# Kernel tuning notes

Hardware: AMD Instinct MI355X
Metric: run time of the kernel (lower is better)

## Reference

```python
import jax, jax.numpy as jnp
import numpy as np

B, HW, NTGT, C = 2, 4096, 4096, 512
H, KNN = 8, 32
DH = C // H
SCALE = DH ** -0.5


def setup_inputs() -> dict:
    key = jax.random.key(0)
    ks = jax.random.split(key, 12)
    s = 1.0 / np.sqrt(C)
    return {
        "src": jax.random.normal(ks[0], (B, HW, C), jnp.float32),
        "tgt": jax.random.normal(ks[1], (B, NTGT, C), jnp.float32),
        "indices": jax.random.randint(ks[2], (B, HW, KNN), 0, NTGT, jnp.int64),
        "weights": jax.random.normal(ks[3], (B, HW, KNN), jnp.float32),
        "Wq": jax.random.normal(ks[4], (C, C), jnp.float32) * s,
        "bq": jnp.zeros((C,), jnp.float32),
        "Wk": jax.random.normal(ks[5], (C, C), jnp.float32) * s,
        "bk": jnp.zeros((C,), jnp.float32),
        "Wv": jax.random.normal(ks[6], (C, C), jnp.float32) * s,
        "bv": jnp.zeros((C,), jnp.float32),
        "Wo": jax.random.normal(ks[7], (C, C), jnp.float32) * s,
        "bo": jnp.zeros((C,), jnp.float32),
    }


def reference(src, tgt, indices, weights, Wq, bq, Wk, bk, Wv, bv, Wo, bo):
    b, hw, c = src.shape
    # projections -> (b, H, seq, dh)
    q = (src @ Wq + bq).reshape(b, hw, H, DH).transpose(0, 2, 1, 3)
    k = (tgt @ Wk + bk).reshape(b, -1, H, DH).transpose(0, 2, 1, 3)
    v = (tgt @ Wv + bv).reshape(b, -1, H, DH).transpose(0, 2, 1, 3)
    # gather epipolar neighbors: per batch, kb[:, idx] -> (H, hw, KNN, dh)
    gather = jax.vmap(lambda xb, ib: xb[:, ib])
    k_g = gather(k, indices)  # (b, H, hw, KNN, dh)
    v_g = gather(v, indices)  # (b, H, hw, KNN, dh)
    logits = jnp.einsum("bhqd,bhqkd->bhqk", q, k_g) * SCALE
    logits = logits + weights[:, None]  # broadcast over heads
    attn = jax.nn.softmax(logits, axis=-1)
    out = jnp.einsum("bhqk,bhqkd->bhqd", attn, v_g)
    out = out.transpose(0, 2, 1, 3).reshape(b, hw, c)
    return out @ Wo + bo
```

## Files before the change

kernel.cpp:

```cpp
#include <hip/hip_runtime.h>
#include <hip/hip_bf16.h>
#include <stdint.h>
#include <type_traits>

#define B_    2
#define HW_   4096
#define NTGT_ 4096
#define C_    512
#define H_    8
#define KNN_  32
#define DH_   64
#define M_    (B_ * HW_)

typedef unsigned short ushort_t;
typedef __bf16 bf16x8 __attribute__((ext_vector_type(8)));
typedef float floatx4 __attribute__((ext_vector_type(4)));

__device__ __forceinline__ float b2f(ushort_t u) {
    union { uint32_t i; float f; } x;
    x.i = ((uint32_t)u) << 16;
    return x.f;
}
__device__ __forceinline__ ushort_t f2b(float f) {
    union { float f; uint32_t i; } x;
    x.f = f;
    uint32_t r = x.i + 0x7fffu + ((x.i >> 16) & 1u);
    return (ushort_t)(r >> 16);
}
__device__ __forceinline__ uint32_t pk2(float x, float y) {
    union { __hip_bfloat162 h2; uint32_t u; } c;
    c.h2 = __float22bfloat162_rn(make_float2(x, y));
    return c.u;
}
__device__ __forceinline__ uint4 pack8(const float4& a, const float4& b) {
    return make_uint4(pk2(a.x, a.y), pk2(a.z, a.w), pk2(b.x, b.y), pk2(b.z, b.w));
}

__global__ __launch_bounds__(256) void transpose_inplace4_f32(
    float* W0, float* W1, float* W2, float* W3) {
    __shared__ float ta[32][33];
    __shared__ float tb[32][33];

    float* W = (blockIdx.y == 0) ? W0 : (blockIdx.y == 1) ? W1
               : (blockIdx.y == 2) ? W2 : W3;

    int p = blockIdx.x;
    int i = 0, acc = 0;
    while (acc + (16 - i) <= p) { acc += 16 - i; ++i; }
    const int j = i + (p - acc);

    const int t = threadIdx.x;
    const int r = t >> 3;
    const int c0 = (t & 7) * 4;

    {
        float4 d = *(const float4*)&W[(size_t)(i * 32 + r) * 512 + j * 32 + c0];
        ta[r][c0 + 0] = d.x; ta[r][c0 + 1] = d.y;
        ta[r][c0 + 2] = d.z; ta[r][c0 + 3] = d.w;
    }
    if (i != j) {
        float4 d = *(const float4*)&W[(size_t)(j * 32 + r) * 512 + i * 32 + c0];
        tb[r][c0 + 0] = d.x; tb[r][c0 + 1] = d.y;
        tb[r][c0 + 2] = d.z; tb[r][c0 + 3] = d.w;
    }
    __syncthreads();

    *(float4*)&W[(size_t)(j * 32 + r) * 512 + i * 32 + c0] =
        make_float4(ta[c0 + 0][r], ta[c0 + 1][r], ta[c0 + 2][r], ta[c0 + 3][r]);
    if (i != j)
        *(float4*)&W[(size_t)(i * 32 + r) * 512 + j * 32 + c0] =
            make_float4(tb[c0 + 0][r], tb[c0 + 1][r], tb[c0 + 2][r], tb[c0 + 3][r]);
}

template <typename AT, typename OT>
__device__ __forceinline__ void gemm_body(const AT* __restrict__ A,
                                          const float* __restrict__ Wt,
                                          const float* __restrict__ bias,
                                          OT* __restrict__ O,
                                          int bm, int bn) {
    __shared__ ushort_t As[128][40];
    __shared__ ushort_t Bs[64][40];

    const int t = threadIdx.x;
    const int lr = t >> 2;
    const int lc = (t & 3) * 8;

    const int lane = t & 63;
    const int wv = t >> 6;
    const int wr = (wv >> 1) * 64;
    const int wc = (wv & 1) * 32;
    const int r16 = lane & 15;
    const int quad = lane >> 4;

    floatx4 acc[4][2] = {};

    for (int kt = 0; kt < 512; kt += 32) {
        uint4 av0, av1, bv0;
        if constexpr (std::is_same<AT, float>::value) {
            const float* p0 = &A[(size_t)(bm + lr) * 512 + kt + lc];
            const float* p1 = &A[(size_t)(bm + lr + 64) * 512 + kt + lc];
            av0 = pack8(*(const float4*)p0, *(const float4*)(p0 + 4));
            av1 = pack8(*(const float4*)p1, *(const float4*)(p1 + 4));
        } else {
            av0 = *(const uint4*)&A[(size_t)(bm + lr) * 512 + kt + lc];
            av1 = *(const uint4*)&A[(size_t)(bm + lr + 64) * 512 + kt + lc];
        }
        {
            const float* p = &Wt[(size_t)(bn + lr) * 512 + kt + lc];
            bv0 = pack8(*(const float4*)p, *(const float4*)(p + 4));
        }
        __syncthreads();
        *(uint4*)&As[lr][lc] = av0;
        *(uint4*)&As[lr + 64][lc] = av1;
        *(uint4*)&Bs[lr][lc] = bv0;
        __syncthreads();

        bf16x8 af[4], bf[2];
#pragma unroll
        for (int i = 0; i < 4; ++i)
            af[i] = *(const bf16x8*)&As[wr + i * 16 + r16][quad * 8];
#pragma unroll
        for (int j = 0; j < 2; ++j)
            bf[j] = *(const bf16x8*)&Bs[wc + j * 16 + r16][quad * 8];
#pragma unroll
        for (int i = 0; i < 4; ++i)
#pragma unroll
            for (int j = 0; j < 2; ++j)
                acc[i][j] = __builtin_amdgcn_mfma_f32_16x16x32_bf16(
                    af[i], bf[j], acc[i][j], 0, 0, 0);
    }

#pragma unroll
    for (int j = 0; j < 2; ++j) {
        const int col = bn + wc + j * 16 + r16;
        const float bj = bias[col];
#pragma unroll
        for (int i = 0; i < 4; ++i) {
            const int row = bm + wr + i * 16 + quad * 4;
#pragma unroll
            for (int r = 0; r < 4; ++r) {
                float v = acc[i][j][r] + bj;
                if constexpr (std::is_same<OT, ushort_t>::value)
                    O[(size_t)(row + r) * 512 + col] = f2b(v);
                else
                    O[(size_t)(row + r) * 512 + col] = v;
            }
        }
    }
}

__global__ __launch_bounds__(256, 4) void gemm_qkv(
    const float* __restrict__ src, const float* __restrict__ tgt,
    const float* __restrict__ WtQ, const float* __restrict__ WtK,
    const float* __restrict__ WtV,
    const float* __restrict__ bq, const float* __restrict__ bk,
    const float* __restrict__ bv,
    ushort_t* __restrict__ Qb, ushort_t* __restrict__ Kb,
    ushort_t* __restrict__ Vb) {
    const int id = blockIdx.x;
    const int xcd = id & 7;
    const int g = id >> 3;
    const int mgrp = g / 24;
    const int r = g % 24;
    const int z = r >> 3;
    const int bn = (r & 7) * 64;
    const int bm = (xcd + 8 * mgrp) * 128;

    const float* A = (z == 0) ? src : tgt;
    const float* Wt = (z == 0) ? WtQ : (z == 1) ? WtK : WtV;
    const float* bias = (z == 0) ? bq : (z == 1) ? bk : bv;
    ushort_t* O = (z == 0) ? Qb : (z == 1) ? Kb : Vb;
    gemm_body<float, ushort_t>(A, Wt, bias, O, bm, bn);
}

template <typename OT>
__global__ __launch_bounds__(256, 4) void gemm_o(const ushort_t* __restrict__ A,
                                                 const float* __restrict__ Wt,
                                                 const float* __restrict__ bias,
                                                 OT* __restrict__ O) {
    const int id = blockIdx.x;
    const int xcd = id & 7;
    const int g = id >> 3;
    const int mgrp = g >> 3;
    const int bn = (g & 7) * 64;
    const int bm = (xcd + 8 * mgrp) * 128;
    gemm_body<ushort_t, OT>(A, Wt, bias, O, bm, bn);
}

#define KVSTRIDE 520
template <typename IT>
__global__ __launch_bounds__(256) void attn_kernel(const ushort_t* Q,
                                                   const ushort_t* __restrict__ K,
                                                   const ushort_t* __restrict__ V,
                                                   const IT* __restrict__ idx,
                                                   const float* __restrict__ wts,
                                                   ushort_t* O) {
    __shared__ float qs[512];
    __shared__ ushort_t kvs[KNN_][KVSTRIDE];
    __shared__ float ps[H_][KNN_];
    __shared__ int idxs[KNN_];
    __shared__ float ws[KNN_];

    const int t = threadIdx.x;
    const int id = blockIdx.x;
    const int xcd = id & 7;
    const int slot = id >> 3;
    const int b = xcd >> 2;
    const int bq = b * HW_ + (xcd & 3) * 1024 + slot;
    const size_t qoff = (size_t)bq * C_;

    {
        uint32_t d = *(const uint32_t*)(Q + qoff + 2 * t);
        qs[2 * t + 0] = b2f((ushort_t)(d & 0xffffu));
        qs[2 * t + 1] = b2f((ushort_t)(d >> 16));
    }
    if (t < KNN_) {
        idxs[t] = (int)idx[(size_t)bq * KNN_ + t];
        ws[t] = wts[(size_t)bq * KNN_ + t];
    }
    __syncthreads();

    const int sr = t >> 3;
    const int sg = (t & 7) * 8;
    {
        const ushort_t* krow = K + ((size_t)(b * NTGT_ + idxs[sr])) * C_;
#pragma unroll
        for (int j = 0; j < 8; ++j)
            *(uint4*)&kvs[sr][sg + j * 64] = *(const uint4*)(krow + sg + j * 64);
    }
    __syncthreads();

    const int h = t >> 5;
    const int n = t & 31;
    const float* qh = qs + h * DH_;
    float dot = 0.f;
#pragma unroll
    for (int j = 0; j < 8; ++j) {
        uint4 kv = *(const uint4*)&kvs[n][h * DH_ + j * 8];
        const int d0 = j * 8;
        dot = fmaf(qh[d0 + 0], b2f((ushort_t)(kv.x & 0xffffu)), dot);
        dot = fmaf(qh[d0 + 1], b2f((ushort_t)(kv.x >> 16)), dot);
        dot = fmaf(qh[d0 + 2], b2f((ushort_t)(kv.y & 0xffffu)), dot);
        dot = fmaf(qh[d0 + 3], b2f((ushort_t)(kv.y >> 16)), dot);
        dot = fmaf(qh[d0 + 4], b2f((ushort_t)(kv.z & 0xffffu)), dot);
        dot = fmaf(qh[d0 + 5], b2f((ushort_t)(kv.z >> 16)), dot);
        dot = fmaf(qh[d0 + 6], b2f((ushort_t)(kv.w & 0xffffu)), dot);
        dot = fmaf(qh[d0 + 7], b2f((ushort_t)(kv.w >> 16)), dot);
    }
    float logit = dot * 0.125f + ws[n];

    float mx = logit;
#pragma unroll
    for (int o = 16; o > 0; o >>= 1) mx = fmaxf(mx, __shfl_xor(mx, o));
    float e = __expf(logit - mx);
    float s = e;
#pragma unroll
    for (int o = 16; o > 0; o >>= 1) s += __shfl_xor(s, o);
    ps[h][n] = e / s;
    __syncthreads();

    {
        const ushort_t* vrow = V + ((size_t)(b * NTGT_ + idxs[sr])) * C_;
#pragma unroll
        for (int j = 0; j < 8; ++j)
            *(uint4*)&kvs[sr][sg + j * 64] = *(const uint4*)(vrow + sg + j * 64);
    }
    __syncthreads();

    const int d2 = (t & 31) * 2;
    float a0 = 0.f, a1 = 0.f;
#pragma unroll 8
    for (int nn = 0; nn < KNN_; ++nn) {
        uint32_t vv = *(const uint32_t*)&kvs[nn][h * DH_ + d2];
        float p = ps[h][nn];
        a0 = fmaf(p, b2f((ushort_t)(vv & 0xffffu)), a0);
        a1 = fmaf(p, b2f((ushort_t)(vv >> 16)), a1);
    }
    *(uint32_t*)(O + qoff + h * DH_ + d2) = pk2(a0, a1);
}

static int elem_bytes(const void* p, size_t n, int dflt) {
    size_t sz = 0;
    hipError_t err = hipPointerGetAttribute(
        &sz, HIP_POINTER_ATTRIBUTE_RANGE_SIZE, (hipDeviceptr_t)(uintptr_t)p);
    if (err == hipSuccess && sz >= n && (sz % n) == 0) {
        size_t b = sz / n;
        if (b == 2 || b == 4 || b == 8) return (int)b;
    }
    return dflt;
}

extern "C" void kernel_launch(void* const* d_in, const int* in_sizes, int n_in,
                              void* d_out, int out_size, void* d_ws, size_t ws_size,
                              hipStream_t stream) {
    const float* src  = (const float*)d_in[0];
    const float* tgt  = (const float*)d_in[1];
    const void*  idxp = d_in[2];
    const float* wtp  = (const float*)d_in[3];
    float* Wq = (float*)d_in[4];  const float* bq = (const float*)d_in[5];
    float* Wk = (float*)d_in[6];  const float* bk = (const float*)d_in[7];
    float* Wv = (float*)d_in[8];  const float* bv = (const float*)d_in[9];
    float* Wo = (float*)d_in[10]; const float* bo = (const float*)d_in[11];

    const size_t NELEM = (size_t)M_ * C_;
    const size_t NIDX  = (size_t)B_ * HW_ * KNN_;

    const int ib = elem_bytes(idxp, NIDX, 4);
    const int ob = elem_bytes(d_out, NELEM, 4);

    dim3 blk(256);

    ushort_t* Qb = (ushort_t*)d_ws;
    ushort_t* Kb = Qb + NELEM;
    ushort_t* Vb = (ushort_t*)d_out;
    ushort_t* Ob = Qb;

    transpose_inplace4_f32<<<dim3(136, 4), blk, 0, stream>>>(Wq, Wk, Wv, Wo);

    gemm_qkv<<<dim3(1536), blk, 0, stream>>>(
        src, tgt, Wq, Wk, Wv, bq, bk, bv, Qb, Kb, Vb);

    if (ib == 8)
        attn_kernel<long long><<<dim3(B_ * HW_), blk, 0, stream>>>(
            Qb, Kb, Vb, (const long long*)idxp, wtp, Ob);
    else
        attn_kernel<int><<<dim3(B_ * HW_), blk, 0, stream>>>(
            Qb, Kb, Vb, (const int*)idxp, wtp, Ob);

    if (ob == 2)
        gemm_o<ushort_t><<<dim3(512), blk, 0, stream>>>(
            Ob, Wo, bo, (ushort_t*)d_out);
    else
        gemm_o<float><<<dim3(512), blk, 0, stream>>>(
            Ob, Wo, bo, (float*)d_out);
}
```

Baseline: 192.7 us.

## Halve GEMM M-tile, prefetch next K-slice in registers, co-issue K/V gathers

The GEMM tile shrinks from 128x64 to 64x64, which doubles the grid size of both the QKV and output projections, and the main loop now register-prefetches the next K-slice while MFMAs run on the current one. In the attention kernel, the gathered V rows are loaded into registers together with the K rows, so their latency overlaps the logit and softmax phase instead of waiting behind a barrier. The trade-offs are more registers per thread and less A-tile reuse per block, which means more global traffic for the weight operand.

New measurement: 282.6 us. +46.7%, slower.

```diff
diff --git a/kernel.cpp b/kernel.cpp
--- a/kernel.cpp
+++ b/kernel.cpp
@@ -78,7 +78,7 @@
                                           const float* __restrict__ bias,
                                           OT* __restrict__ O,
                                           int bm, int bn) {
-    __shared__ ushort_t As[128][40];
+    __shared__ ushort_t As[64][40];
     __shared__ ushort_t Bs[64][40];
 
     const int t = threadIdx.x;
@@ -87,47 +87,55 @@
 
     const int lane = t & 63;
     const int wv = t >> 6;
-    const int wr = (wv >> 1) * 64;
+    const int wr = (wv >> 1) * 32;
     const int wc = (wv & 1) * 32;
     const int r16 = lane & 15;
     const int quad = lane >> 4;
 
-    floatx4 acc[4][2] = {};
+    floatx4 acc[2][2] = {};
+
+    float4 fa0, fa1, fb0, fb1;
+    uint4 ua;
+
+    if constexpr (std::is_same<AT, float>::value) {
+        const float* p = &A[(size_t)(bm + lr) * 512 + lc];
+        fa0 = *(const float4*)p; fa1 = *(const float4*)(p + 4);
+    } else {
+        ua = *(const uint4*)&A[(size_t)(bm + lr) * 512 + lc];
+    }
+    {
+        const float* p = &Wt[(size_t)(bn + lr) * 512 + lc];
+        fb0 = *(const float4*)p; fb1 = *(const float4*)(p + 4);
+    }
 
     for (int kt = 0; kt < 512; kt += 32) {
-        uint4 av0, av1, bv0;
-        if constexpr (std::is_same<AT, float>::value) {
-            const float* p0 = &A[(size_t)(bm + lr) * 512 + kt + lc];
-            const float* p1 = &A[(size_t)(bm + lr + 64) * 512 + kt + lc];
-            av0 = pack8(*(const float4*)p0, *(const float4*)(p0 + 4));
-            av1 = pack8(*(const float4*)p1, *(const float4*)(p1 + 4));
-        } else {
-            av0 = *(const uint4*)&A[(size_t)(bm + lr) * 512 + kt + lc];
-            av1 = *(const uint4*)&A[(size_t)(bm + lr + 64) * 512 + kt + lc];
+        __syncthreads();
+        if constexpr (std::is_same<AT, float>::value)
+            *(uint4*)&As[lr][lc] = pack8(fa0, fa1);
+        else
+            *(uint4*)&As[lr][lc] = ua;
+        *(uint4*)&Bs[lr][lc] = pack8(fb0, fb1);
+        __syncthreads();
+
+        if (kt + 32 < 512) {
+            if constexpr (std::is_same<AT, float>::value) {
+                const float* p = &A[(size_t)(bm + lr) * 512 + kt + 32 + lc];
+                fa0 = *(const float4*)p; fa1 = *(const float4*)(p + 4);
+            } else {
+                ua = *(const uint4*)&A[(size_t)(bm + lr) * 512 + kt + 32 + lc];
+            }
+            const float* p = &Wt[(size_t)(bn + lr) * 512 + kt + 32 + lc];
+            fb0 = *(const float4*)p; fb1 = *(const float4*)(p + 4);
         }
-        {
-            const float* p = &Wt[(size_t)(bn + lr) * 512 + kt + lc];
-            bv0 = pack8(*(const float4*)p, *(const float4*)(p + 4));
-        }
-        __syncthreads();
-        *(uint4*)&As[lr][lc] = av0;
-        *(uint4*)&As[lr + 64][lc] = av1;
-        *(uint4*)&Bs[lr][lc] = bv0;
-        __syncthreads();
-
-        bf16x8 af[4], bf[2];
-#pragma unroll
-        for (int i = 0; i < 4; ++i)
-            af[i] = *(const bf16x8*)&As[wr + i * 16 + r16][quad * 8];
-#pragma unroll
-        for (int j = 0; j < 2; ++j)
-            bf[j] = *(const bf16x8*)&Bs[wc + j * 16 + r16][quad * 8];
-#pragma unroll
-        for (int i = 0; i < 4; ++i)
-#pragma unroll
-            for (int j = 0; j < 2; ++j)
-                acc[i][j] = __builtin_amdgcn_mfma_f32_16x16x32_bf16(
-                    af[i], bf[j], acc[i][j], 0, 0, 0);
+
+        bf16x8 a0 = *(const bf16x8*)&As[wr + r16][quad * 8];
+        bf16x8 a1 = *(const bf16x8*)&As[wr + 16 + r16][quad * 8];
+        bf16x8 b0 = *(const bf16x8*)&Bs[wc + r16][quad * 8];
+        bf16x8 b1 = *(const bf16x8*)&Bs[wc + 16 + r16][quad * 8];
+        acc[0][0] = __builtin_amdgcn_mfma_f32_16x16x32_bf16(a0, b0, acc[0][0], 0, 0, 0);
+        acc[0][1] = __builtin_amdgcn_mfma_f32_16x16x32_bf16(a0, b1, acc[0][1], 0, 0, 0);
+        acc[1][0] = __builtin_amdgcn_mfma_f32_16x16x32_bf16(a1, b0, acc[1][0], 0, 0, 0);
+        acc[1][1] = __builtin_amdgcn_mfma_f32_16x16x32_bf16(a1, b1, acc[1][1], 0, 0, 0);
     }
 
 #pragma unroll
@@ -135,7 +143,7 @@
         const int col = bn + wc + j * 16 + r16;
         const float bj = bias[col];
 #pragma unroll
-        for (int i = 0; i < 4; ++i) {
+        for (int i = 0; i < 2; ++i) {
             const int row = bm + wr + i * 16 + quad * 4;
 #pragma unroll
             for (int r = 0; r < 4; ++r) {
@@ -164,7 +172,7 @@
     const int r = g % 24;
     const int z = r >> 3;
     const int bn = (r & 7) * 64;
-    const int bm = (xcd + 8 * mgrp) * 128;
+    const int bm = (xcd + 8 * mgrp) * 64;
 
     const float* A = (z == 0) ? src : tgt;
     const float* Wt = (z == 0) ? WtQ : (z == 1) ? WtK : WtV;
@@ -183,7 +191,7 @@
     const int g = id >> 3;
     const int mgrp = g >> 3;
     const int bn = (g & 7) * 64;
-    const int bm = (xcd + 8 * mgrp) * 128;
+    const int bm = (xcd + 8 * mgrp) * 64;
     gemm_body<ushort_t, OT>(A, Wt, bias, O, bm, bn);
 }
 
@@ -222,12 +230,14 @@
 
     const int sr = t >> 3;
     const int sg = (t & 7) * 8;
-    {
-        const ushort_t* krow = K + ((size_t)(b * NTGT_ + idxs[sr])) * C_;
-#pragma unroll
-        for (int j = 0; j < 8; ++j)
-            *(uint4*)&kvs[sr][sg + j * 64] = *(const uint4*)(krow + sg + j * 64);
-    }
+    const size_t roff = ((size_t)(b * NTGT_ + idxs[sr])) * C_;
+    uint4 kr[8], vr[8];
+#pragma unroll
+    for (int j = 0; j < 8; ++j) kr[j] = *(const uint4*)(K + roff + sg + j * 64);
+#pragma unroll
+    for (int j = 0; j < 8; ++j) vr[j] = *(const uint4*)(V + roff + sg + j * 64);
+#pragma unroll
+    for (int j = 0; j < 8; ++j) *(uint4*)&kvs[sr][sg + j * 64] = kr[j];
     __syncthreads();
 
     const int h = t >> 5;
@@ -259,12 +269,8 @@
     ps[h][n] = e / s;
     __syncthreads();
 
-    {
-        const ushort_t* vrow = V + ((size_t)(b * NTGT_ + idxs[sr])) * C_;
-#pragma unroll
-        for (int j = 0; j < 8; ++j)
-            *(uint4*)&kvs[sr][sg + j * 64] = *(const uint4*)(vrow + sg + j * 64);
-    }
+#pragma unroll
+    for (int j = 0; j < 8; ++j) *(uint4*)&kvs[sr][sg + j * 64] = vr[j];
     __syncthreads();
 
     const int d2 = (t & 31) * 2;
@@ -317,7 +323,7 @@
 
     transpose_inplace4_f32<<<dim3(136, 4), blk, 0, stream>>>(Wq, Wk, Wv, Wo);
 
-    gemm_qkv<<<dim3(1536), blk, 0, stream>>>(
+    gemm_qkv<<<dim3(3072), blk, 0, stream>>>(
         src, tgt, Wq, Wk, Wv, bq, bk, bv, Qb, Kb, Vb);
 
     if (ib == 8)
@@ -328,9 +334,9 @@
             Qb, Kb, Vb, (const int*)idxp, wtp, Ob);
 
     if (ob == 2)
-        gemm_o<ushort_t><<<dim3(512), blk, 0, stream>>>(
+        gemm_o<ushort_t><<<dim3(1024), blk, 0, stream>>>(
             Ob, Wo, bo, (ushort_t*)d_out);
     else
-        gemm_o<float><<<dim3(512), blk, 0, stream>>>(
+        gemm_o<float><<<dim3(1024), blk, 0, stream>>>(
             Ob, Wo, bo, (float*)d_out);
 }
```

## Pretranspose weights to bf16 workspace, prefetch GEMM tiles, widen QKV N-tile

Applied to the files above, without the earlier changes.

Weights are now transposed and converted to bf16 once into workspace, out of place, instead of being transposed in place as fp32. The GEMM body register-prefetches the next K-slice from global memory while MFMAs run on the current one, which drops one barrier per iteration. The QKV GEMM uses a 128-wide N tile with fewer blocks and launch bounds of 3. The aim is to halve weight traffic, hide load latency and raise reuse of A, at the cost of more registers and lower occupancy.

Measured after the change: 191.7 us. About the same (-0.5%).

```diff
diff --git a/kernel.cpp b/kernel.cpp
--- a/kernel.cpp
+++ b/kernel.cpp
@@ -36,6 +36,35 @@
     return make_uint4(pk2(a.x, a.y), pk2(a.z, a.w), pk2(b.x, b.y), pk2(b.z, b.w));
 }
 
+__global__ __launch_bounds__(256) void transpose_cvt4(
+    const float* __restrict__ W0, const float* __restrict__ W1,
+    const float* __restrict__ W2, const float* __restrict__ W3,
+    ushort_t* __restrict__ T0, ushort_t* __restrict__ T1,
+    ushort_t* __restrict__ T2, ushort_t* __restrict__ T3) {
+    __shared__ float tile[32][33];
+
+    const float* W = (blockIdx.z == 0) ? W0 : (blockIdx.z == 1) ? W1
+                     : (blockIdx.z == 2) ? W2 : W3;
+    ushort_t* T = (blockIdx.z == 0) ? T0 : (blockIdx.z == 1) ? T1
+                  : (blockIdx.z == 2) ? T2 : T3;
+
+    const int k0 = blockIdx.x * 32;
+    const int n0 = blockIdx.y * 32;
+    const int t = threadIdx.x;
+    const int r = t >> 3;
+    const int c0 = (t & 7) * 4;
+
+    float4 d = *(const float4*)&W[(size_t)(k0 + r) * 512 + n0 + c0];
+    tile[r][c0 + 0] = d.x; tile[r][c0 + 1] = d.y;
+    tile[r][c0 + 2] = d.z; tile[r][c0 + 3] = d.w;
+    __syncthreads();
+
+    uint2 o;
+    o.x = pk2(tile[c0 + 0][r], tile[c0 + 1][r]);
+    o.y = pk2(tile[c0 + 2][r], tile[c0 + 3][r]);
+    *(uint2*)&T[(size_t)(n0 + r) * 512 + k0 + c0] = o;
+}
+
 __global__ __launch_bounds__(256) void transpose_inplace4_f32(
     float* W0, float* W1, float* W2, float* W3) {
     __shared__ float ta[32][33];
@@ -72,14 +101,15 @@
             make_float4(tb[c0 + 0][r], tb[c0 + 1][r], tb[c0 + 2][r], tb[c0 + 3][r]);
 }
 
-template <typename AT, typename OT>
+template <typename AT, typename BT, typename OT, int BN>
 __device__ __forceinline__ void gemm_body(const AT* __restrict__ A,
-                                          const float* __restrict__ Wt,
+                                          const BT* __restrict__ Wt,
                                           const float* __restrict__ bias,
                                           OT* __restrict__ O,
                                           int bm, int bn) {
+    constexpr int NJ = BN / 32;
     __shared__ ushort_t As[128][40];
-    __shared__ ushort_t Bs[64][40];
+    __shared__ ushort_t Bs[BN][40];
 
     const int t = threadIdx.x;
     const int lr = t >> 2;
@@ -88,50 +118,97 @@
     const int lane = t & 63;
     const int wv = t >> 6;
     const int wr = (wv >> 1) * 64;
-    const int wc = (wv & 1) * 32;
+    const int wc = (wv & 1) * (BN / 2);
     const int r16 = lane & 15;
     const int quad = lane >> 4;
 
-    floatx4 acc[4][2] = {};
+    floatx4 acc[4][NJ] = {};
+
+    float4 fa0, fa1, fa2, fa3, fb0, fb1, fb2, fb3;
+    uint4 ua0, ua1, ub0, ub1;
+
+    if constexpr (std::is_same<AT, float>::value) {
+        const float* p0 = &A[(size_t)(bm + lr) * 512 + lc];
+        const float* p1 = &A[(size_t)(bm + lr + 64) * 512 + lc];
+        fa0 = *(const float4*)p0; fa1 = *(const float4*)(p0 + 4);
+        fa2 = *(const float4*)p1; fa3 = *(const float4*)(p1 + 4);
+    } else {
+        ua0 = *(const uint4*)&A[(size_t)(bm + lr) * 512 + lc];
+        ua1 = *(const uint4*)&A[(size_t)(bm + lr + 64) * 512 + lc];
+    }
+    if constexpr (std::is_same<BT, float>::value) {
+        const float* p0 = &Wt[(size_t)(bn + lr) * 512 + lc];
+        fb0 = *(const float4*)p0; fb1 = *(const float4*)(p0 + 4);
+        if constexpr (BN == 128) {
+            const float* p1 = &Wt[(size_t)(bn + lr + 64) * 512 + lc];
+            fb2 = *(const float4*)p1; fb3 = *(const float4*)(p1 + 4);
+        }
+    } else {
+        ub0 = *(const uint4*)&Wt[(size_t)(bn + lr) * 512 + lc];
+        if constexpr (BN == 128)
+            ub1 = *(const uint4*)&Wt[(size_t)(bn + lr + 64) * 512 + lc];
+    }
 
     for (int kt = 0; kt < 512; kt += 32) {
-        uint4 av0, av1, bv0;
+        __syncthreads();
         if constexpr (std::is_same<AT, float>::value) {
-            const float* p0 = &A[(size_t)(bm + lr) * 512 + kt + lc];
-            const float* p1 = &A[(size_t)(bm + lr + 64) * 512 + kt + lc];
-            av0 = pack8(*(const float4*)p0, *(const float4*)(p0 + 4));
-            av1 = pack8(*(const float4*)p1, *(const float4*)(p1 + 4));
+            *(uint4*)&As[lr][lc] = pack8(fa0, fa1);
+            *(uint4*)&As[lr + 64][lc] = pack8(fa2, fa3);
         } else {
-            av0 = *(const uint4*)&A[(size_t)(bm + lr) * 512 + kt + lc];
-            av1 = *(const uint4*)&A[(size_t)(bm + lr + 64) * 512 + kt + lc];
+            *(uint4*)&As[lr][lc] = ua0;
+            *(uint4*)&As[lr + 64][lc] = ua1;
         }
-        {
-            const float* p = &Wt[(size_t)(bn + lr) * 512 + kt + lc];
-            bv0 = pack8(*(const float4*)p, *(const float4*)(p + 4));
+        if constexpr (std::is_same<BT, float>::value) {
+            *(uint4*)&Bs[lr][lc] = pack8(fb0, fb1);
+            if constexpr (BN == 128) *(uint4*)&Bs[lr + 64][lc] = pack8(fb2, fb3);
+        } else {
+            *(uint4*)&Bs[lr][lc] = ub0;
+            if constexpr (BN == 128) *(uint4*)&Bs[lr + 64][lc] = ub1;
         }
         __syncthreads();
-        *(uint4*)&As[lr][lc] = av0;
-        *(uint4*)&As[lr + 64][lc] = av1;
-        *(uint4*)&Bs[lr][lc] = bv0;
-        __syncthreads();
-
-        bf16x8 af[4], bf[2];
+
+        if (kt + 32 < 512) {
+            const int k2 = kt + 32;
+            if constexpr (std::is_same<AT, float>::value) {
+                const float* p0 = &A[(size_t)(bm + lr) * 512 + k2 + lc];
+                const float* p1 = &A[(size_t)(bm + lr + 64) * 512 + k2 + lc];
+                fa0 = *(const float4*)p0; fa1 = *(const float4*)(p0 + 4);
+                fa2 = *(const float4*)p1; fa3 = *(const float4*)(p1 + 4);
+            } else {
+                ua0 = *(const uint4*)&A[(size_t)(bm + lr) * 512 + k2 + lc];
+                ua1 = *(const uint4*)&A[(size_t)(bm + lr + 64) * 512 + k2 + lc];
+            }
+            if constexpr (std::is_same<BT, float>::value) {
+                const float* p0 = &Wt[(size_t)(bn + lr) * 512 + k2 + lc];
+                fb0 = *(const float4*)p0; fb1 = *(const float4*)(p0 + 4);
+                if constexpr (BN == 128) {
+                    const float* p1 = &Wt[(size_t)(bn + lr + 64) * 512 + k2 + lc];
+                    fb2 = *(const float4*)p1; fb3 = *(const float4*)(p1 + 4);
+                }
+            } else {
+                ub0 = *(const uint4*)&Wt[(size_t)(bn + lr) * 512 + k2 + lc];
+                if constexpr (BN == 128)
+                    ub1 = *(const uint4*)&Wt[(size_t)(bn + lr + 64) * 512 + k2 + lc];
+            }
+        }
+
+        bf16x8 af[4], bf[NJ];
 #pragma unroll
         for (int i = 0; i < 4; ++i)
             af[i] = *(const bf16x8*)&As[wr + i * 16 + r16][quad * 8];
 #pragma unroll
-        for (int j = 0; j < 2; ++j)
+        for (int j = 0; j < NJ; ++j)
             bf[j] = *(const bf16x8*)&Bs[wc + j * 16 + r16][quad * 8];
 #pragma unroll
         for (int i = 0; i < 4; ++i)
 #pragma unroll
-            for (int j = 0; j < 2; ++j)
+            for (int j = 0; j < NJ; ++j)
                 acc[i][j] = __builtin_amdgcn_mfma_f32_16x16x32_bf16(
                     af[i], bf[j], acc[i][j], 0, 0, 0);
     }
 
 #pragma unroll
-    for (int j = 0; j < 2; ++j) {
+    for (int j = 0; j < NJ; ++j) {
         const int col = bn + wc + j * 16 + r16;
         const float bj = bias[col];
 #pragma unroll
@@ -149,10 +226,11 @@
     }
 }
 
-__global__ __launch_bounds__(256, 4) void gemm_qkv(
+template <typename BT>
+__global__ __launch_bounds__(256, 3) void gemm_qkv(
     const float* __restrict__ src, const float* __restrict__ tgt,
-    const float* __restrict__ WtQ, const float* __restrict__ WtK,
-    const float* __restrict__ WtV,
+    const BT* __restrict__ WtQ, const BT* __restrict__ WtK,
+    const BT* __restrict__ WtV,
     const float* __restrict__ bq, const float* __restrict__ bk,
     const float* __restrict__ bv,
     ushort_t* __restrict__ Qb, ushort_t* __restrict__ Kb,
@@ -160,22 +238,22 @@
     const int id = blockIdx.x;
     const int xcd = id & 7;
     const int g = id >> 3;
-    const int mgrp = g / 24;
-    const int r = g % 24;
-    const int z = r >> 3;
-    const int bn = (r & 7) * 64;
+    const int mgrp = g / 12;
+    const int r = g % 12;
+    const int z = r >> 2;
+    const int bn = (r & 3) * 128;
     const int bm = (xcd + 8 * mgrp) * 128;
 
     const float* A = (z == 0) ? src : tgt;
-    const float* Wt = (z == 0) ? WtQ : (z == 1) ? WtK : WtV;
+    const BT* Wt = (z == 0) ? WtQ : (z == 1) ? WtK : WtV;
     const float* bias = (z == 0) ? bq : (z == 1) ? bk : bv;
     ushort_t* O = (z == 0) ? Qb : (z == 1) ? Kb : Vb;
-    gemm_body<float, ushort_t>(A, Wt, bias, O, bm, bn);
-}
-
-template <typename OT>
+    gemm_body<float, BT, ushort_t, 128>(A, Wt, bias, O, bm, bn);
+}
+
+template <typename BT, typename OT>
 __global__ __launch_bounds__(256, 4) void gemm_o(const ushort_t* __restrict__ A,
-                                                 const float* __restrict__ Wt,
+                                                 const BT* __restrict__ Wt,
                                                  const float* __restrict__ bias,
                                                  OT* __restrict__ O) {
     const int id = blockIdx.x;
@@ -184,7 +262,7 @@
     const int mgrp = g >> 3;
     const int bn = (g & 7) * 64;
     const int bm = (xcd + 8 * mgrp) * 128;
-    gemm_body<ushort_t, OT>(A, Wt, bias, O, bm, bn);
+    gemm_body<ushort_t, BT, OT, 64>(A, Wt, bias, O, bm, bn);
 }
 
 #define KVSTRIDE 520
@@ -303,6 +381,7 @@
     float* Wo = (float*)d_in[10]; const float* bo = (const float*)d_in[11];
 
     const size_t NELEM = (size_t)M_ * C_;
+    const size_t WELEM = (size_t)C_ * C_;
     const size_t NIDX  = (size_t)B_ * HW_ * KNN_;
 
     const int ib = elem_bytes(idxp, NIDX, 4);
@@ -315,22 +394,52 @@
     ushort_t* Vb = (ushort_t*)d_out;
     ushort_t* Ob = Qb;
 
-    transpose_inplace4_f32<<<dim3(136, 4), blk, 0, stream>>>(Wq, Wk, Wv, Wo);
-
-    gemm_qkv<<<dim3(1536), blk, 0, stream>>>(
-        src, tgt, Wq, Wk, Wv, bq, bk, bv, Qb, Kb, Vb);
-
-    if (ib == 8)
-        attn_kernel<long long><<<dim3(B_ * HW_), blk, 0, stream>>>(
-            Qb, Kb, Vb, (const long long*)idxp, wtp, Ob);
-    else
-        attn_kernel<int><<<dim3(B_ * HW_), blk, 0, stream>>>(
-            Qb, Kb, Vb, (const int*)idxp, wtp, Ob);
-
-    if (ob == 2)
-        gemm_o<ushort_t><<<dim3(512), blk, 0, stream>>>(
-            Ob, Wo, bo, (ushort_t*)d_out);
-    else
-        gemm_o<float><<<dim3(512), blk, 0, stream>>>(
-            Ob, Wo, bo, (float*)d_out);
-}
+    const bool wfit = ws_size >= (2 * NELEM + 4 * WELEM) * sizeof(ushort_t);
+
+    if (wfit) {
+        ushort_t* T = Kb + NELEM;
+        ushort_t* WtQ = T;
+        ushort_t* WtK = T + WELEM;
+        ushort_t* WtV = T + 2 * WELEM;
+        ushort_t* WtO = T + 3 * WELEM;
+
+        transpose_cvt4<<<dim3(16, 16, 4), blk, 0, stream>>>(
+            Wq, Wk, Wv, Wo, WtQ, WtK, WtV, WtO);
+
+        gemm_qkv<ushort_t><<<dim3(768), blk, 0, stream>>>(
+            src, tgt, WtQ, WtK, WtV, bq, bk, bv, Qb, Kb, Vb);
+
+        if (ib == 8)
+            attn_kernel<long long><<<dim3(B_ * HW_), blk, 0, stream>>>(
+                Qb, Kb, Vb, (const long long*)idxp, wtp, Ob);
+        else
+            attn_kernel<int><<<dim3(B_ * HW_), blk, 0, stream>>>(
+                Qb, Kb, Vb, (const int*)idxp, wtp, Ob);
+
+        if (ob == 2)
+            gemm_o<ushort_t, ushort_t><<<dim3(512), blk, 0, stream>>>(
+                Ob, WtO, bo, (ushort_t*)d_out);
+        else
+            gemm_o<ushort_t, float><<<dim3(512), blk, 0, stream>>>(
+                Ob, WtO, bo, (float*)d_out);
+    } else {
+        transpose_inplace4_f32<<<dim3(136, 4), blk, 0, stream>>>(Wq, Wk, Wv, Wo);
+
+        gemm_qkv<float><<<dim3(768), blk, 0, stream>>>(
+            src, tgt, Wq, Wk, Wv, bq, bk, bv, Qb, Kb, Vb);
+
+        if (ib == 8)
+            attn_kernel<long long><<<dim3(B_ * HW_), blk, 0, stream>>>(
+                Qb, Kb, Vb, (const long long*)idxp, wtp, Ob);
+        else
+            attn_kernel<int><<<dim3(B_ * HW_), blk, 0, stream>>>(
+                Qb, Kb, Vb, (const int*)idxp, wtp, Ob);
+
+        if (ob == 2)
+            gemm_o<float, ushort_t><<<dim3(512), blk, 0, stream>>>(
+                Ob, Wo, bo, (ushort_t*)d_out);
+        else
+            gemm_o<float, float><<<dim3(512), blk, 0, stream>>>(
+                Ob, Wo, bo, (float*)d_out);
+    }
+}
```
